# Optimization experiments

Measured on AMD Instinct MI355X. Metric: run time of the kernel, lower is better.

The kernel has to match this reference:

```python
import jax, jax.numpy as jnp
import numpy as np

B, N, DOP, DM, H = 8, 2048, 256, 256, 256  # batch, n_ops==n_machines, dims


def setup_inputs() -> dict:
    key = jax.random.key(0)
    ks = jax.random.split(key, 21)
    s = 0.02
    inp = {
        "operation_features": jax.random.normal(ks[0], (B, N, DOP), jnp.float32),
        "machine_features": jax.random.normal(ks[1], (B, N, DM), jnp.float32),
        "type_match_mask": jax.random.bernoulli(ks[2], 0.3, (B, N, N)).astype(jnp.float32),
        "same_type_mask": jax.random.bernoulli(ks[3], 0.3, (B, N, N)).astype(jnp.float32),
        "oma_q_w": jax.random.normal(ks[4], (H, DM), jnp.float32) * s,
        "oma_q_b": jnp.zeros((H,), jnp.float32),
        "oma_kv_w": jax.random.normal(ks[5], (2 * H, DOP), jnp.float32) * s,
        "oma_kv_b": jnp.zeros((2 * H,), jnp.float32),
        "oma_s_w": jax.random.normal(ks[6], (1, 2 * H), jnp.float32) * s,
        "oma_s_b": jnp.zeros((1,), jnp.float32),
        "oma_o_w": jax.random.normal(ks[7], (DM, H), jnp.float32) * s,
        "oma_o_b": jnp.zeros((DM,), jnp.float32),
        "sa_w_w": jax.random.normal(ks[8], (3 * H, DM), jnp.float32) * s,
        "sa_w_b": jnp.zeros((3 * H,), jnp.float32),
        "sa_s_w": jax.random.normal(ks[9], (1, 2 * H), jnp.float32) * s,
        "sa_s_b": jnp.zeros((1,), jnp.float32),
        "sa_o_w": jax.random.normal(ks[10], (DM, H), jnp.float32) * s,
        "sa_o_b": jnp.zeros((DM,), jnp.float32),
        "mix_w": jax.random.normal(ks[11], (DM, 2 * DM), jnp.float32) * s,
        "mix_b": jnp.zeros((DM,), jnp.float32),
    }
    return inp


def reference(operation_features, machine_features, type_match_mask, same_type_mask,
              oma_q_w, oma_q_b, oma_kv_w, oma_kv_b, oma_s_w, oma_s_b, oma_o_w, oma_o_b,
              sa_w_w, sa_w_b, sa_s_w, sa_s_b, sa_o_w, sa_o_b, mix_w, mix_b):
    # --- OperationMachineAttention ---
    q = machine_features @ oma_q_w.T + oma_q_b            # (B,M,H)
    kv = operation_features @ oma_kv_w.T + oma_kv_b       # (B,C,2H)
    k, v = jnp.split(kv, 2, axis=-1)
    # Linear(cat([q,k])) == q @ W[:, :H].T + k @ W[:, H:].T + b (additive-score factorization)
    sq = jnp.einsum('bmh,h->bm', q, oma_s_w[0, :H])
    sk = jnp.einsum('bch,h->bc', k, oma_s_w[0, H:])
    scores = jax.nn.leaky_relu(sq[:, :, None] + sk[:, None, :] + oma_s_b[0])  # (B,M,C)
    p = jax.nn.softmax(scores * type_match_mask, axis=-1)
    wf = jnp.einsum('bmc,bch->bmh', p, v)
    operation_machine = wf @ oma_o_w.T + oma_o_b           # (B,M,DM)

    # --- SelfAttention over machines ---
    w3 = machine_features @ sa_w_w.T + sa_w_b              # (B,C,3H)
    q2, k2, v2 = jnp.split(w3, 3, axis=-1)
    sq2 = jnp.einsum('bih,h->bi', q2, sa_s_w[0, :H])
    sk2 = jnp.einsum('bjh,h->bj', k2, sa_s_w[0, H:])
    s2 = jax.nn.leaky_relu(sq2[:, :, None] + sk2[:, None, :] + sa_s_b[0])  # (B,C,C)
    p2 = jax.nn.softmax(s2 * same_type_mask, axis=-1)
    machine_machine = jnp.einsum('bij,bjh->bih', p2, v2) @ sa_o_w.T + sa_o_b  # (B,C,DM)

    # --- mix ---
    mixed = jnp.concatenate([operation_machine, machine_machine], axis=-1)
    return mixed @ mix_w.T + mix_b                          # (B,N,DM)
```

## Files before the change

kernel.cpp:

```cpp
#include <hip/hip_runtime.h>
#include <stdint.h>
#include <stddef.h>

#define B_ 8
#define N_ 2048
#define C_ 2048
#define D_ 256
#define H_ 256

typedef __bf16 bf16x8 __attribute__((ext_vector_type(8)));
typedef __bf16 bf16x4 __attribute__((ext_vector_type(4)));
typedef float f32x4 __attribute__((ext_vector_type(4)));

#define MFMA16(a, b, c) __builtin_amdgcn_mfma_f32_16x16x32_bf16((a), (b), (c), 0, 0, 0)

__global__ __launch_bounds__(256) void k0a_partial(
    const float* __restrict__ oma_q_w, const float* __restrict__ oma_kv_w,
    const float* __restrict__ sa_w_w,
    const float* __restrict__ oma_s_w, const float* __restrict__ sa_s_w,
    float* __restrict__ partial)
{
    int d = threadIdx.x;
    int vec = blockIdx.x >> 3, hc = blockIdx.x & 7;
    int h0 = hc * 32;
    const float* Wb; const float* sv;
    if (vec == 0)      { Wb = oma_q_w  + h0 * 256;         sv = oma_s_w + h0; }
    else if (vec == 1) { Wb = oma_kv_w + h0 * 256;         sv = oma_s_w + 256 + h0; }
    else if (vec == 2) { Wb = sa_w_w   + h0 * 256;         sv = sa_s_w + h0; }
    else               { Wb = sa_w_w   + (256 + h0) * 256; sv = sa_s_w + 256 + h0; }
    float a = 0.f;
    #pragma unroll 8
    for (int h = 0; h < 32; ++h) a += Wb[h * 256 + d] * sv[h];
    partial[blockIdx.x * 256 + d] = a;
}

__global__ __launch_bounds__(256) void k0b_reduce(
    const float* __restrict__ partial,
    const float* __restrict__ oma_q_b, const float* __restrict__ oma_kv_b,
    const float* __restrict__ oma_s_w, const float* __restrict__ oma_s_b,
    const float* __restrict__ sa_w_b, const float* __restrict__ sa_s_w,
    const float* __restrict__ sa_s_b,
    float* __restrict__ wq_v, float* __restrict__ wk_v,
    float* __restrict__ wq2_v, float* __restrict__ wk2_v,
    float* __restrict__ sb)
{
    int d = threadIdx.x;
    float a0 = 0.f, a1 = 0.f, a2 = 0.f, a3 = 0.f;
    #pragma unroll
    for (int hc = 0; hc < 8; ++hc) {
        a0 += partial[(0 * 8 + hc) * 256 + d];
        a1 += partial[(1 * 8 + hc) * 256 + d];
        a2 += partial[(2 * 8 + hc) * 256 + d];
        a3 += partial[(3 * 8 + hc) * 256 + d];
    }
    wq_v[d] = a0; wk_v[d] = a1; wq2_v[d] = a2; wk2_v[d] = a3;

    int h = d;
    float p1 = oma_q_b[h] * oma_s_w[h] + oma_kv_b[h] * oma_s_w[256 + h];
    float p2 = sa_w_b[h] * sa_s_w[h] + sa_w_b[256 + h] * sa_s_w[256 + h];
    for (int o = 32; o; o >>= 1) { p1 += __shfl_xor(p1, o); p2 += __shfl_xor(p2, o); }
    __shared__ float redA[4], redB[4];
    int wv = threadIdx.x >> 6;
    if ((threadIdx.x & 63) == 0) { redA[wv] = p1; redB[wv] = p2; }
    __syncthreads();
    if (threadIdx.x == 0) {
        sb[0] = redA[0] + redA[1] + redA[2] + redA[3] + oma_s_b[0];
        sb[1] = redB[0] + redB[1] + redB[2] + redB[3] + sa_s_b[0];
    }
}

__global__ __launch_bounds__(256) void k1_wcat(
    const float* __restrict__ mix_w, const float* __restrict__ mix_b,
    const float* __restrict__ oma_o_w, const float* __restrict__ oma_o_b,
    const float* __restrict__ sa_o_w, const float* __restrict__ sa_o_b,
    __bf16* __restrict__ Wcat, float* __restrict__ b_total)
{
    int d = blockIdx.x, h = threadIdx.x;
    const float* mwr = mix_w + d * 512;
    float w1 = 0.f, w2 = 0.f;
    #pragma unroll 4
    for (int e = 0; e < 256; ++e) {
        w1 += mwr[e] * oma_o_w[e * 256 + h];
        w2 += mwr[256 + e] * sa_o_w[e * 256 + h];
    }
    Wcat[d * 512 + h] = (__bf16)w1;
    Wcat[d * 512 + 256 + h] = (__bf16)w2;

    float pb = mwr[h] * oma_o_b[h] + mwr[256 + h] * sa_o_b[h];
    for (int o = 32; o; o >>= 1) pb += __shfl_xor(pb, o);
    __shared__ float red[4];
    if ((h & 63) == 0) red[h >> 6] = pb;
    __syncthreads();
    if (h == 0) b_total[d] = mix_b[d] + red[0] + red[1] + red[2] + red[3];
}

__global__ __launch_bounds__(256) void k2_scores(
    const float* __restrict__ op, const float* __restrict__ mach,
    const float* __restrict__ wq_v, const float* __restrict__ wk_v,
    const float* __restrict__ wq2_v, const float* __restrict__ wk2_v,
    const float* __restrict__ sb,
    float* __restrict__ sqp, float* __restrict__ skv,
    float* __restrict__ sq2p, float* __restrict__ sk2v)
{
    int t = threadIdx.x, lane = t & 63, wv = t >> 6;
    size_t n = (size_t)blockIdx.x * 4 + wv;
    const float4 mf = *(const float4*)(mach + n * 256 + lane * 4);
    const float4 of = *(const float4*)(op + n * 256 + lane * 4);
    const float4 q4 = *(const float4*)(wq_v + lane * 4);
    const float4 k4 = *(const float4*)(wk_v + lane * 4);
    const float4 q24 = *(const float4*)(wq2_v + lane * 4);
    const float4 k24 = *(const float4*)(wk2_v + lane * 4);
    float s1 = mf.x * q4.x + mf.y * q4.y + mf.z * q4.z + mf.w * q4.w;
    float s2 = of.x * k4.x + of.y * k4.y + of.z * k4.z + of.w * k4.w;
    float s3 = mf.x * q24.x + mf.y * q24.y + mf.z * q24.z + mf.w * q24.w;
    float s4 = mf.x * k24.x + mf.y * k24.y + mf.z * k24.z + mf.w * k24.w;
    for (int o = 32; o; o >>= 1) {
        s1 += __shfl_xor(s1, o); s2 += __shfl_xor(s2, o);
        s3 += __shfl_xor(s3, o); s4 += __shfl_xor(s4, o);
    }
    if (lane == 0) {
        sqp[n] = s1 + sb[0]; skv[n] = s2;
        sq2p[n] = s3 + sb[1]; sk2v[n] = s4;
    }
}

__global__ __launch_bounds__(256, 2) void k3_vgemm(
    const float* __restrict__ op, const float* __restrict__ mach,
    const float* __restrict__ oma_kv_w, const float* __restrict__ sa_w_w,
    __bf16* __restrict__ vt)
{
    __shared__ __attribute__((aligned(16))) __bf16 As[64][72];
    __shared__ __attribute__((aligned(16))) __bf16 Bs[64][72];
    int t = threadIdx.x;
    int bid = blockIdx.x;
    int which = bid >> 10;
    int r = bid & 1023;
    int b = r >> 7;
    int ht = (r >> 5) & 3;
    int ct = r & 31;

    const float* Aglob = (which ? (sa_w_w + 512 * 256) : (oma_kv_w + 256 * 256)) + ht * 64 * 256;
    const float* Bglob = (which ? mach : op) + ((size_t)b * N_ + ct * 64) * 256;

    int lane = t & 63, wv = t >> 6;
    int l15 = lane & 15, qo = (lane >> 4) * 8;
    int rr = t >> 4;
    int dd = (t & 15) * 4;

    f32x4 acc[4] = {};

    for (int d0 = 0; d0 < 256; d0 += 64) {
        #pragma unroll
        for (int p = 0; p < 4; ++p) {
            float4 av = *(const float4*)(Aglob + (size_t)(p * 16 + rr) * 256 + d0 + dd);
            float4 bv = *(const float4*)(Bglob + (size_t)(p * 16 + rr) * 256 + d0 + dd);
            bf16x4 a4, b4;
            a4[0] = (__bf16)av.x; a4[1] = (__bf16)av.y; a4[2] = (__bf16)av.z; a4[3] = (__bf16)av.w;
            b4[0] = (__bf16)bv.x; b4[1] = (__bf16)bv.y; b4[2] = (__bf16)bv.z; b4[3] = (__bf16)bv.w;
            *(bf16x4*)&As[p * 16 + rr][dd] = a4;
            *(bf16x4*)&Bs[p * 16 + rr][dd] = b4;
        }
        __syncthreads();
        #pragma unroll
        for (int kb = 0; kb < 2; ++kb) {
            bf16x8 bfr = *(const bf16x8*)&Bs[16 * wv + l15][kb * 32 + qo];
            #pragma unroll
            for (int rt = 0; rt < 4; ++rt) {
                bf16x8 afr = *(const bf16x8*)&As[16 * rt + l15][kb * 32 + qo];
                acc[rt] = MFMA16(afr, bfr, acc[rt]);
            }
        }
        __syncthreads();
    }
    #pragma unroll
    for (int rt = 0; rt < 4; ++rt)
        #pragma unroll
        for (int j = 0; j < 4; ++j)
            As[16 * rt + (lane >> 4) * 4 + j][16 * wv + l15] = (__bf16)acc[rt][j];
    __syncthreads();
    int hh = t >> 2, cb = (t & 3) * 16;
    __bf16* orow = vt + (((size_t)(which * 8 + b)) * 256 + ht * 64 + hh) * 2048 + ct * 64 + cb;
    *(bf16x8*)(orow) = *(const bf16x8*)&As[hh][cb];
    *(bf16x8*)(orow + 8) = *(const bf16x8*)&As[hh][cb + 8];
}

__device__ __forceinline__ f32x4 ntload4f(const float* p) {
    return __builtin_nontemporal_load(reinterpret_cast<const f32x4*>(p));
}

__global__ __launch_bounds__(256, 2) void k4_attn(
    const float* __restrict__ tmask, const float* __restrict__ smask,
    const float* __restrict__ sqp, const float* __restrict__ skv,
    const float* __restrict__ sq2p, const float* __restrict__ sk2v,
    const __bf16* __restrict__ vt,
    __bf16* __restrict__ wfcat)
{
    __shared__ __attribute__((aligned(16))) __bf16 eA[64][72];
    __shared__ __attribute__((aligned(16))) __bf16 vB[256][72];
    __shared__ uint16_t Mb[64 * 130];
    __shared__ float rowsum[64];

    int t = threadIdx.x;
    int bid = blockIdx.x;
    int wg = (bid & 7) * 64 + (bid >> 3);
    int which = wg >> 8;
    int r = wg & 255;
    int b = r >> 5;
    int m0 = (r & 31) * 64;

    const float* mask = (which ? smask : tmask) + ((size_t)b * N_ + m0) * C_;
    const float* sqrow = (which ? sq2p : sqp) + b * N_ + m0;
    const float* skrow = (which ? sk2v : skv) + b * N_;
    const __bf16* vbase = vt + ((size_t)(which * 8 + b)) * 256 * 2048;

    int lane = t & 63, wv = t >> 6;
    int l15 = lane & 15, qo = (lane >> 4) * 8;
    int mrow = t >> 2;
    int cq16 = (t & 3) * 16;
    int vh = t >> 3;
    int vc = (t & 7) * 8;

    float sqv = sqrow[mrow];
    float psum = 0.f;
    f32x4 acc[4][4] = {};

    bf16x8 vv[8];
    f32x4 skc[4];

    auto load_v = [&](int c0) {
        #pragma unroll
        for (int p = 0; p < 8; ++p)
            vv[p] = *(const bf16x8*)(vbase + (size_t)(p * 32 + vh) * 2048 + c0 + vc);
    };
    auto load_sk = [&](int c0) {
        #pragma unroll
        for (int i = 0; i < 4; ++i) skc[i] = *(const f32x4*)(skrow + c0 + cq16 + 4 * i);
    };

    load_v(0);
    load_sk(0);

    {
        int tcol = t & 127;
        int trow = t >> 7;
        const float* mb = mask + (size_t)trow * C_ + tcol * 16;
        #pragma unroll 4
        for (int i = 0; i < 32; ++i) {
            const float* p = mb + (size_t)i * 2 * C_;
            f32x4 a = ntload4f(p);
            f32x4 bq = ntload4f(p + 4);
            f32x4 cq = ntload4f(p + 8);
            f32x4 dq = ntload4f(p + 12);
            uint32_t bits = 0;
            #pragma unroll
            for (int j = 0; j < 4; ++j) {
                bits |= (a[j]  != 0.f ? 1u : 0u) << j;
                bits |= (bq[j] != 0.f ? 1u : 0u) << (4 + j);
                bits |= (cq[j] != 0.f ? 1u : 0u) << (8 + j);
                bits |= (dq[j] != 0.f ? 1u : 0u) << (12 + j);
            }
            Mb[(i * 2 + trow) * 130 + tcol] = (uint16_t)bits;
        }
    }
    __syncthreads();

    #pragma unroll 1
    for (int c0 = 0; c0 < C_; c0 += 64) {
        #pragma unroll
        for (int p = 0; p < 8; ++p)
            *(bf16x8*)&vB[p * 32 + vh][vc] = vv[p];
        uint32_t mbits = Mb[mrow * 130 + (c0 >> 4) + (t & 3)];
        bf16x8 e0, e1;
        #pragma unroll
        for (int i = 0; i < 16; ++i) {
            float s = sqv + skc[i >> 2][i & 3];
            s = s > 0.f ? s : 0.01f * s;
            float e = (mbits & (1u << i)) ? __expf(s) : 1.0f;
            psum += e;
            if (i < 8) e0[i] = (__bf16)e; else e1[i - 8] = (__bf16)e;
        }
        *(bf16x8*)&eA[mrow][cq16] = e0;
        *(bf16x8*)&eA[mrow][cq16 + 8] = e1;
        __syncthreads();
        int cn = c0 + 64; if (cn >= C_) cn = 0;
        load_v(cn);
        load_sk(cn);
        #pragma unroll
        for (int kb = 0; kb < 2; ++kb) {
            bf16x8 afr[4];
            #pragma unroll
            for (int rt = 0; rt < 4; ++rt)
                afr[rt] = *(const bf16x8*)&eA[16 * rt + l15][kb * 32 + qo];
            #pragma unroll
            for (int ctile = 0; ctile < 4; ++ctile) {
                bf16x8 bfr = *(const bf16x8*)&vB[64 * wv + 16 * ctile + l15][kb * 32 + qo];
                #pragma unroll
                for (int rt = 0; rt < 4; ++rt)
                    acc[rt][ctile] = MFMA16(afr[rt], bfr, acc[rt][ctile]);
            }
        }
        __syncthreads();
    }

    float rs = psum;
    rs += __shfl_xor(rs, 1);
    rs += __shfl_xor(rs, 2);
    if ((t & 3) == 0) rowsum[mrow] = rs;
    __syncthreads();

    __bf16* obuf = &vB[0][0];
    #pragma unroll
    for (int rt = 0; rt < 4; ++rt) {
        #pragma unroll
        for (int j = 0; j < 4; ++j) {
            int m = 16 * rt + (lane >> 4) * 4 + j;
            float inv = __builtin_amdgcn_rcpf(rowsum[m]);
            #pragma unroll
            for (int ctile = 0; ctile < 4; ++ctile)
                obuf[m * 264 + 64 * wv + 16 * ctile + l15] = (__bf16)(acc[rt][ctile][j] * inv);
        }
    }
    __syncthreads();
    int m = t >> 2, cb = (t & 3) * 64;
    __bf16* wrow = wfcat + ((size_t)(b * N_ + m0 + m)) * 512 + which * 256 + cb;
    #pragma unroll
    for (int k = 0; k < 8; ++k)
        *(bf16x8*)(wrow + k * 8) = *(const bf16x8*)&obuf[m * 264 + cb + k * 8];
}

__global__ __launch_bounds__(256, 2) void k5_out(
    const __bf16* __restrict__ wfcat, const __bf16* __restrict__ Wcat,
    const float* __restrict__ b_total, float* __restrict__ out)
{
    __shared__ __attribute__((aligned(16))) __bf16 As[32][72];
    __shared__ __attribute__((aligned(16))) __bf16 Bs[256][72];
    __shared__ float bias[256];
    int t = threadIdx.x;
    int n0 = blockIdx.x * 32;
    int lane = t & 63, wv = t >> 6, l15 = lane & 15, qo = (lane >> 4) * 8;
    bias[t] = b_total[t];
    int ar = t >> 3;
    int ac = (t & 7) * 8;
    f32x4 acc[2][4] = {};

    for (int k0 = 0; k0 < 512; k0 += 64) {
        *(bf16x8*)&As[ar][ac] =
            *(const bf16x8*)(wfcat + (size_t)(n0 + ar) * 512 + k0 + ac);
        #pragma unroll
        for (int p = 0; p < 8; ++p)
            *(bf16x8*)&Bs[p * 32 + ar][ac] =
                *(const bf16x8*)(Wcat + (size_t)(p * 32 + ar) * 512 + k0 + ac);
        __syncthreads();
        #pragma unroll
        for (int kb = 0; kb < 2; ++kb) {
            bf16x8 afr[2];
            #pragma unroll
            for (int rt = 0; rt < 2; ++rt)
                afr[rt] = *(const bf16x8*)&As[16 * rt + l15][kb * 32 + qo];
            #pragma unroll
            for (int ct = 0; ct < 4; ++ct) {
                bf16x8 bfr = *(const bf16x8*)&Bs[64 * wv + 16 * ct + l15][kb * 32 + qo];
                #pragma unroll
                for (int rt = 0; rt < 2; ++rt)
                    acc[rt][ct] = MFMA16(afr[rt], bfr, acc[rt][ct]);
            }
        }
        __syncthreads();
    }
    #pragma unroll
    for (int rt = 0; rt < 2; ++rt) {
        #pragma unroll
        for (int ct = 0; ct < 4; ++ct) {
            int d = 64 * wv + 16 * ct + l15;
            float bv = bias[d];
            #pragma unroll
            for (int j = 0; j < 4; ++j) {
                int m = 16 * rt + (lane >> 4) * 4 + j;
                out[(size_t)(n0 + m) * 256 + d] = acc[rt][ct][j] + bv;
            }
        }
    }
}

extern "C" void kernel_launch(void* const* d_in, const int* in_sizes, int n_in,
                              void* d_out, int out_size, void* d_ws, size_t ws_size,
                              hipStream_t stream)
{
    const float* op_feat  = (const float*)d_in[0];
    const float* mach_feat= (const float*)d_in[1];
    const float* tmask    = (const float*)d_in[2];
    const float* smask    = (const float*)d_in[3];
    const float* oma_q_w  = (const float*)d_in[4];
    const float* oma_q_b  = (const float*)d_in[5];
    const float* oma_kv_w = (const float*)d_in[6];
    const float* oma_kv_b = (const float*)d_in[7];
    const float* oma_s_w  = (const float*)d_in[8];
    const float* oma_s_b  = (const float*)d_in[9];
    const float* oma_o_w  = (const float*)d_in[10];
    const float* oma_o_b  = (const float*)d_in[11];
    const float* sa_w_w   = (const float*)d_in[12];
    const float* sa_w_b   = (const float*)d_in[13];
    const float* sa_s_w   = (const float*)d_in[14];
    const float* sa_s_b   = (const float*)d_in[15];
    const float* sa_o_w   = (const float*)d_in[16];
    const float* sa_o_b   = (const float*)d_in[17];
    const float* mix_w    = (const float*)d_in[18];
    const float* mix_b    = (const float*)d_in[19];

    char* ws = (char*)d_ws;
    float* wq_v   = (float*)(ws + 0);
    float* wk_v   = (float*)(ws + 1024);
    float* wq2_v  = (float*)(ws + 2048);
    float* wk2_v  = (float*)(ws + 3072);
    float* sb     = (float*)(ws + 4096);
    float* btot   = (float*)(ws + 4352);
    float* sqp    = (float*)(ws + 8192);
    float* skv    = (float*)(ws + 73728);
    float* sq2p   = (float*)(ws + 139264);
    float* sk2v   = (float*)(ws + 204800);
    __bf16* Wcat  = (__bf16*)(ws + 270336);
    __bf16* vt    = (__bf16*)(ws + 532480);
    __bf16* wfcat = (__bf16*)(ws + 17309696);
    float* outp   = (float*)d_out;

    float* partial = (float*)(ws + 532480);

    k0a_partial<<<32, 256, 0, stream>>>(oma_q_w, oma_kv_w, sa_w_w,
                                        oma_s_w, sa_s_w, partial);
    k0b_reduce<<<1, 256, 0, stream>>>(partial, oma_q_b, oma_kv_b, oma_s_w, oma_s_b,
                                      sa_w_b, sa_s_w, sa_s_b,
                                      wq_v, wk_v, wq2_v, wk2_v, sb);
    k1_wcat<<<256, 256, 0, stream>>>(mix_w, mix_b, oma_o_w, oma_o_b,
                                     sa_o_w, sa_o_b, Wcat, btot);
    k2_scores<<<4096, 256, 0, stream>>>(op_feat, mach_feat, wq_v, wk_v, wq2_v, wk2_v,
                                        sb, sqp, skv, sq2p, sk2v);
    k3_vgemm<<<2048, 256, 0, stream>>>(op_feat, mach_feat, oma_kv_w, sa_w_w, vt);
    k4_attn<<<512, 256, 0, stream>>>(tmask, smask, sqp, skv, sq2p, sk2v, vt, wfcat);
    k5_out<<<512, 256, 0, stream>>>(wfcat, Wcat, btot, outp);
}
```

Before: 469.2 us.

## Rework weight-fold GEMM, widen V-projection tiles, and stream masks directly in attention

The mix/output weight fold moves from a scalar dot-product kernel to an MFMA tiled GEMM, with the bias fold split into its own small kernel. The V-projection kernel now computes all four H tiles per block, so each activation tile is loaded and converted once instead of four times. The attention kernel drops the shared-memory bitmask precompute and its XCD-aware block remapping. It now loads float mask tiles per chunk and computes exp(s*mask) directly. That adds per-thread mask register traffic and removes the interleaved block swizzle, which may change cache locality.

```diff
diff --git a/kernel.cpp b/kernel.cpp
--- a/kernel.cpp
+++ b/kernel.cpp
@@ -69,29 +69,87 @@
     }
 }
 
-__global__ __launch_bounds__(256) void k1_wcat(
+__global__ __launch_bounds__(256, 2) void k1_wcat(
+    const float* __restrict__ mix_w,
+    const float* __restrict__ oma_o_w, const float* __restrict__ sa_o_w,
+    __bf16* __restrict__ Wcat)
+{
+    __shared__ __attribute__((aligned(16))) __bf16 As[64][72];
+    __shared__ __attribute__((aligned(16))) __bf16 Bs[64][72];
+    int t = threadIdx.x;
+    int dt = blockIdx.x >> 3;
+    int kt = blockIdx.x & 7;
+    int half = kt >> 2;
+    const float* O = half ? sa_o_w : oma_o_w;
+    int kO = (kt & 3) * 64;
+    int d0 = dt * 64;
+    int aeoff = half * 256;
+
+    int lane = t & 63, wv = t >> 6;
+    int l15 = lane & 15, qo = (lane >> 4) * 8;
+    int rr = t >> 4;
+    int dd = (t & 15) * 4;
+    int klane = t & 63;
+    int eq = t >> 6;
+
+    f32x4 acc[4] = {};
+
+    for (int e0 = 0; e0 < 256; e0 += 64) {
+        #pragma unroll
+        for (int p = 0; p < 4; ++p) {
+            float4 av = *(const float4*)(mix_w + (size_t)(d0 + p * 16 + rr) * 512 + aeoff + e0 + dd);
+            bf16x4 a4;
+            a4[0] = (__bf16)av.x; a4[1] = (__bf16)av.y; a4[2] = (__bf16)av.z; a4[3] = (__bf16)av.w;
+            *(bf16x4*)&As[p * 16 + rr][dd] = a4;
+        }
+        #pragma unroll
+        for (int i = 0; i < 16; ++i) {
+            int e_loc = i * 4 + eq;
+            float v = O[(size_t)(e0 + e_loc) * 256 + kO + klane];
+            Bs[klane][e_loc] = (__bf16)v;
+        }
+        __syncthreads();
+        #pragma unroll
+        for (int kb = 0; kb < 2; ++kb) {
+            bf16x8 bfr = *(const bf16x8*)&Bs[16 * wv + l15][kb * 32 + qo];
+            #pragma unroll
+            for (int rt = 0; rt < 4; ++rt) {
+                bf16x8 afr = *(const bf16x8*)&As[16 * rt + l15][kb * 32 + qo];
+                acc[rt] = MFMA16(afr, bfr, acc[rt]);
+            }
+        }
+        __syncthreads();
+    }
+    #pragma unroll
+    for (int rt = 0; rt < 4; ++rt)
+        #pragma unroll
+        for (int j = 0; j < 4; ++j)
+            As[16 * rt + (lane >> 4) * 4 + j][16 * wv + l15] = (__bf16)acc[rt][j];
+    __syncthreads();
+    int hh = t >> 2, cb = (t & 3) * 16;
+    __bf16* orow = Wcat + (size_t)(d0 + hh) * 512 + kt * 64 + cb;
+    *(bf16x8*)(orow) = *(const bf16x8*)&As[hh][cb];
+    *(bf16x8*)(orow + 8) = *(const bf16x8*)&As[hh][cb + 8];
+}
+
+__global__ __launch_bounds__(256) void k1b_bias(
     const float* __restrict__ mix_w, const float* __restrict__ mix_b,
-    const float* __restrict__ oma_o_w, const float* __restrict__ oma_o_b,
-    const float* __restrict__ sa_o_w, const float* __restrict__ sa_o_b,
-    __bf16* __restrict__ Wcat, float* __restrict__ b_total)
-{
-    int d = blockIdx.x, h = threadIdx.x;
+    const float* __restrict__ oma_o_b, const float* __restrict__ sa_o_b,
+    float* __restrict__ b_total)
+{
+    int d = threadIdx.x;
     const float* mwr = mix_w + d * 512;
-    float w1 = 0.f, w2 = 0.f;
+    float s = 0.f;
     #pragma unroll 4
-    for (int e = 0; e < 256; ++e) {
-        w1 += mwr[e] * oma_o_w[e * 256 + h];
-        w2 += mwr[256 + e] * sa_o_w[e * 256 + h];
-    }
-    Wcat[d * 512 + h] = (__bf16)w1;
-    Wcat[d * 512 + 256 + h] = (__bf16)w2;
-
-    float pb = mwr[h] * oma_o_b[h] + mwr[256 + h] * sa_o_b[h];
-    for (int o = 32; o; o >>= 1) pb += __shfl_xor(pb, o);
-    __shared__ float red[4];
-    if ((h & 63) == 0) red[h >> 6] = pb;
-    __syncthreads();
-    if (h == 0) b_total[d] = mix_b[d] + red[0] + red[1] + red[2] + red[3];
+    for (int h = 0; h < 64; ++h) {
+        f32x4 m0 = *(const f32x4*)(mwr + h * 4);
+        f32x4 m1 = *(const f32x4*)(mwr + 256 + h * 4);
+        f32x4 b0 = *(const f32x4*)(oma_o_b + h * 4);
+        f32x4 b1 = *(const f32x4*)(sa_o_b + h * 4);
+        #pragma unroll
+        for (int j = 0; j < 4; ++j) s += m0[j] * b0[j] + m1[j] * b1[j];
+    }
+    b_total[d] = mix_b[d] + s;
 }
 
 __global__ __launch_bounds__(256) void k2_scores(
@@ -129,17 +187,16 @@
     const float* __restrict__ oma_kv_w, const float* __restrict__ sa_w_w,
     __bf16* __restrict__ vt)
 {
-    __shared__ __attribute__((aligned(16))) __bf16 As[64][72];
+    __shared__ __attribute__((aligned(16))) __bf16 As[256][72];
     __shared__ __attribute__((aligned(16))) __bf16 Bs[64][72];
     int t = threadIdx.x;
     int bid = blockIdx.x;
-    int which = bid >> 10;
-    int r = bid & 1023;
-    int b = r >> 7;
-    int ht = (r >> 5) & 3;
+    int which = bid >> 8;
+    int r = bid & 255;
+    int b = r >> 5;
     int ct = r & 31;
 
-    const float* Aglob = (which ? (sa_w_w + 512 * 256) : (oma_kv_w + 256 * 256)) + ht * 64 * 256;
+    const float* Aglob = which ? (sa_w_w + 512 * 256) : (oma_kv_w + 256 * 256);
     const float* Bglob = (which ? mach : op) + ((size_t)b * N_ + ct * 64) * 256;
 
     int lane = t & 63, wv = t >> 6;
@@ -147,17 +204,21 @@
     int rr = t >> 4;
     int dd = (t & 15) * 4;
 
-    f32x4 acc[4] = {};
+    f32x4 acc[4][4] = {};
 
     for (int d0 = 0; d0 < 256; d0 += 64) {
         #pragma unroll
+        for (int p = 0; p < 16; ++p) {
+            float4 av = *(const float4*)(Aglob + (size_t)(p * 16 + rr) * 256 + d0 + dd);
+            bf16x4 a4;
+            a4[0] = (__bf16)av.x; a4[1] = (__bf16)av.y; a4[2] = (__bf16)av.z; a4[3] = (__bf16)av.w;
+            *(bf16x4*)&As[p * 16 + rr][dd] = a4;
+        }
+        #pragma unroll
         for (int p = 0; p < 4; ++p) {
-            float4 av = *(const float4*)(Aglob + (size_t)(p * 16 + rr) * 256 + d0 + dd);
             float4 bv = *(const float4*)(Bglob + (size_t)(p * 16 + rr) * 256 + d0 + dd);
-            bf16x4 a4, b4;
-            a4[0] = (__bf16)av.x; a4[1] = (__bf16)av.y; a4[2] = (__bf16)av.z; a4[3] = (__bf16)av.w;
+            bf16x4 b4;
             b4[0] = (__bf16)bv.x; b4[1] = (__bf16)bv.y; b4[2] = (__bf16)bv.z; b4[3] = (__bf16)bv.w;
-            *(bf16x4*)&As[p * 16 + rr][dd] = a4;
             *(bf16x4*)&Bs[p * 16 + rr][dd] = b4;
         }
         __syncthreads();
@@ -165,27 +226,29 @@
         for (int kb = 0; kb < 2; ++kb) {
             bf16x8 bfr = *(const bf16x8*)&Bs[16 * wv + l15][kb * 32 + qo];
             #pragma unroll
-            for (int rt = 0; rt < 4; ++rt) {
-                bf16x8 afr = *(const bf16x8*)&As[16 * rt + l15][kb * 32 + qo];
-                acc[rt] = MFMA16(afr, bfr, acc[rt]);
-            }
-        }
-        __syncthreads();
-    }
-    #pragma unroll
-    for (int rt = 0; rt < 4; ++rt)
-        #pragma unroll
-        for (int j = 0; j < 4; ++j)
-            As[16 * rt + (lane >> 4) * 4 + j][16 * wv + l15] = (__bf16)acc[rt][j];
-    __syncthreads();
+            for (int ht = 0; ht < 4; ++ht)
+                #pragma unroll
+                for (int rt = 0; rt < 4; ++rt) {
+                    bf16x8 afr = *(const bf16x8*)&As[ht * 64 + 16 * rt + l15][kb * 32 + qo];
+                    acc[ht][rt] = MFMA16(afr, bfr, acc[ht][rt]);
+                }
+        }
+        __syncthreads();
+    }
     int hh = t >> 2, cb = (t & 3) * 16;
-    __bf16* orow = vt + (((size_t)(which * 8 + b)) * 256 + ht * 64 + hh) * 2048 + ct * 64 + cb;
-    *(bf16x8*)(orow) = *(const bf16x8*)&As[hh][cb];
-    *(bf16x8*)(orow + 8) = *(const bf16x8*)&As[hh][cb + 8];
-}
-
-__device__ __forceinline__ f32x4 ntload4f(const float* p) {
-    return __builtin_nontemporal_load(reinterpret_cast<const f32x4*>(p));
+    #pragma unroll 1
+    for (int ht = 0; ht < 4; ++ht) {
+        #pragma unroll
+        for (int rt = 0; rt < 4; ++rt)
+            #pragma unroll
+            for (int j = 0; j < 4; ++j)
+                Bs[16 * rt + (lane >> 4) * 4 + j][16 * wv + l15] = (__bf16)acc[ht][rt][j];
+        __syncthreads();
+        __bf16* orow = vt + (((size_t)(which * 8 + b)) * 256 + ht * 64 + hh) * 2048 + ct * 64 + cb;
+        *(bf16x8*)(orow) = *(const bf16x8*)&Bs[hh][cb];
+        *(bf16x8*)(orow + 8) = *(const bf16x8*)&Bs[hh][cb + 8];
+        __syncthreads();
+    }
 }
 
 __global__ __launch_bounds__(256, 2) void k4_attn(
@@ -197,14 +260,12 @@
 {
     __shared__ __attribute__((aligned(16))) __bf16 eA[64][72];
     __shared__ __attribute__((aligned(16))) __bf16 vB[256][72];
-    __shared__ uint16_t Mb[64 * 130];
     __shared__ float rowsum[64];
 
     int t = threadIdx.x;
     int bid = blockIdx.x;
-    int wg = (bid & 7) * 64 + (bid >> 3);
-    int which = wg >> 8;
-    int r = wg & 255;
+    int which = bid >> 8;
+    int r = bid & 255;
     int b = r >> 5;
     int m0 = (r & 31) * 64;
 
@@ -216,7 +277,7 @@
     int lane = t & 63, wv = t >> 6;
     int l15 = lane & 15, qo = (lane >> 4) * 8;
     int mrow = t >> 2;
-    int cq16 = (t & 3) * 16;
+    int cqb = (t & 3) * 16;
     int vh = t >> 3;
     int vc = (t & 7) * 8;
 
@@ -225,66 +286,40 @@
     f32x4 acc[4][4] = {};
 
     bf16x8 vv[8];
-    f32x4 skc[4];
-
-    auto load_v = [&](int c0) {
+    float mk[16], skc[16];
+
+    auto load_tiles = [&](int c0) {
         #pragma unroll
         for (int p = 0; p < 8; ++p)
             vv[p] = *(const bf16x8*)(vbase + (size_t)(p * 32 + vh) * 2048 + c0 + vc);
+        #pragma unroll
+        for (int i = 0; i < 4; ++i) {
+            float4 m4 = *(const float4*)(mask + (size_t)mrow * C_ + c0 + cqb + i * 4);
+            float4 s4 = *(const float4*)(skrow + c0 + cqb + i * 4);
+            mk[4 * i + 0] = m4.x; mk[4 * i + 1] = m4.y; mk[4 * i + 2] = m4.z; mk[4 * i + 3] = m4.w;
+            skc[4 * i + 0] = s4.x; skc[4 * i + 1] = s4.y; skc[4 * i + 2] = s4.z; skc[4 * i + 3] = s4.w;
+        }
     };
-    auto load_sk = [&](int c0) {
-        #pragma unroll
-        for (int i = 0; i < 4; ++i) skc[i] = *(const f32x4*)(skrow + c0 + cq16 + 4 * i);
-    };
-
-    load_v(0);
-    load_sk(0);
-
-    {
-        int tcol = t & 127;
-        int trow = t >> 7;
-        const float* mb = mask + (size_t)trow * C_ + tcol * 16;
-        #pragma unroll 4
-        for (int i = 0; i < 32; ++i) {
-            const float* p = mb + (size_t)i * 2 * C_;
-            f32x4 a = ntload4f(p);
-            f32x4 bq = ntload4f(p + 4);
-            f32x4 cq = ntload4f(p + 8);
-            f32x4 dq = ntload4f(p + 12);
-            uint32_t bits = 0;
-            #pragma unroll
-            for (int j = 0; j < 4; ++j) {
-                bits |= (a[j]  != 0.f ? 1u : 0u) << j;
-                bits |= (bq[j] != 0.f ? 1u : 0u) << (4 + j);
-                bits |= (cq[j] != 0.f ? 1u : 0u) << (8 + j);
-                bits |= (dq[j] != 0.f ? 1u : 0u) << (12 + j);
-            }
-            Mb[(i * 2 + trow) * 130 + tcol] = (uint16_t)bits;
-        }
-    }
-    __syncthreads();
-
-    #pragma unroll 1
+    load_tiles(0);
+
     for (int c0 = 0; c0 < C_; c0 += 64) {
         #pragma unroll
         for (int p = 0; p < 8; ++p)
             *(bf16x8*)&vB[p * 32 + vh][vc] = vv[p];
-        uint32_t mbits = Mb[mrow * 130 + (c0 >> 4) + (t & 3)];
         bf16x8 e0, e1;
         #pragma unroll
         for (int i = 0; i < 16; ++i) {
-            float s = sqv + skc[i >> 2][i & 3];
+            float s = sqv + skc[i];
             s = s > 0.f ? s : 0.01f * s;
-            float e = (mbits & (1u << i)) ? __expf(s) : 1.0f;
+            float e = __expf(s * mk[i]);
             psum += e;
             if (i < 8) e0[i] = (__bf16)e; else e1[i - 8] = (__bf16)e;
         }
-        *(bf16x8*)&eA[mrow][cq16] = e0;
-        *(bf16x8*)&eA[mrow][cq16 + 8] = e1;
+        *(bf16x8*)&eA[mrow][cqb] = e0;
+        *(bf16x8*)&eA[mrow][cqb + 8] = e1;
         __syncthreads();
         int cn = c0 + 64; if (cn >= C_) cn = 0;
-        load_v(cn);
-        load_sk(cn);
+        load_tiles(cn);
         #pragma unroll
         for (int kb = 0; kb < 2; ++kb) {
             bf16x8 afr[4];
@@ -430,11 +465,11 @@
     k0b_reduce<<<1, 256, 0, stream>>>(partial, oma_q_b, oma_kv_b, oma_s_w, oma_s_b,
                                       sa_w_b, sa_s_w, sa_s_b,
                                       wq_v, wk_v, wq2_v, wk2_v, sb);
-    k1_wcat<<<256, 256, 0, stream>>>(mix_w, mix_b, oma_o_w, oma_o_b,
-                                     sa_o_w, sa_o_b, Wcat, btot);
+    k1_wcat<<<32, 256, 0, stream>>>(mix_w, oma_o_w, sa_o_w, Wcat);
+    k1b_bias<<<1, 256, 0, stream>>>(mix_w, mix_b, oma_o_b, sa_o_b, btot);
     k2_scores<<<4096, 256, 0, stream>>>(op_feat, mach_feat, wq_v, wk_v, wq2_v, wk2_v,
                                         sb, sqp, skv, sq2p, sk2v);
-    k3_vgemm<<<2048, 256, 0, stream>>>(op_feat, mach_feat, oma_kv_w, sa_w_w, vt);
+    k3_vgemm<<<512, 256, 0, stream>>>(op_feat, mach_feat, oma_kv_w, sa_w_w, vt);
     k4_attn<<<512, 256, 0, stream>>>(tmask, smask, sqp, skv, sq2p, sk2v, vt, wfcat);
     k5_out<<<512, 256, 0, stream>>>(wfcat, Wcat, btot, outp);
 }
```

Result: slower. 519.7 us (+10.8%).
